# Kernel tuning notes

Hardware: AMD Instinct MI355X
Metric: run time of the kernel (lower is better)

The kernel has to match this reference:

```python
import jax, jax.numpy as jnp
import numpy as np

B, S, D, H = 4, 2048, 1024, 16
HD = D // H


def setup_inputs() -> dict:
    key = jax.random.key(0)
    ks = jax.random.split(key, 6)
    s = 1.0 / np.sqrt(D)
    return {
        "x": jax.random.normal(ks[0], (B, S, D), dtype=jnp.float32),
        "Wq": jax.random.normal(ks[1], (D, D), dtype=jnp.float32) * s,
        "Wk": jax.random.normal(ks[2], (D, D), dtype=jnp.float32) * s,
        "Wv": jax.random.normal(ks[3], (D, D), dtype=jnp.float32) * s,
        "Wo": jax.random.normal(ks[4], (D, D), dtype=jnp.float32) * s,
        "bo": jnp.zeros((D,), dtype=jnp.float32),
    }


def reference(x, Wq, Wk, Wv, Wo, bo):
    b, n, d = x.shape
    # QKV projections (torch Linear: x @ W.T, but weights here are stored as [d_in, d_out])
    q = (x @ Wq).reshape(b, n, H, HD).transpose(0, 2, 1, 3)  # [b,h,n,hd]
    k = (x @ Wk).reshape(b, n, H, HD).transpose(0, 2, 1, 3)
    v = (x @ Wv).reshape(b, n, H, HD).transpose(0, 2, 1, 3)
    scores = jnp.einsum("bhqd,bhkd->bhqk", q, k) / np.sqrt(HD)
    causal = jnp.tril(jnp.ones((n, n), dtype=bool))  # True = keep
    scores = jnp.where(causal, scores, -jnp.inf)
    attn = jax.nn.softmax(scores, axis=-1)
    ctx = jnp.einsum("bhqk,bhkd->bhqd", attn, v)
    ctx = ctx.transpose(0, 2, 1, 3).reshape(b, n, d)
    return ctx @ Wo + bo
```

## Files before the change

### kernel.cpp

```cpp
#include <hip/hip_runtime.h>
#include <hip/hip_bf16.h>

typedef __bf16 bf16;
typedef __bf16 bf16x4 __attribute__((ext_vector_type(4)));
typedef __bf16 bf16x8 __attribute__((ext_vector_type(8)));
typedef float f32x4 __attribute__((ext_vector_type(4)));

static constexpr int Bn = 4, Sn = 2048, Dn = 1024, Hn = 16, HDn = 64;
static constexpr int Mn = Bn * Sn;

__device__ __forceinline__ void gload_lds16(const void* g, void* l) {
  __builtin_amdgcn_global_load_lds(
      (const __attribute__((address_space(1))) unsigned int*)g,
      (__attribute__((address_space(3))) unsigned int*)l, 16, 0, 0);
}

struct alignas(8) B4 { bf16 e[4]; };

__global__ void prep_kernel(const float* __restrict__ x, bf16* __restrict__ xb,
                            const float* __restrict__ W0, const float* __restrict__ W1,
                            const float* __restrict__ W2, const float* __restrict__ W3,
                            bf16* __restrict__ WtQKV, bf16* __restrict__ Wot) {
  const int bid = blockIdx.x;
  if (bid < 4096) {
    const int i = bid * 256 + threadIdx.x;
    const float4* p = reinterpret_cast<const float4*>(x) + (size_t)i * 2;
    float4 a = p[0], b = p[1];
    bf16x8 v;
    v[0] = (bf16)a.x; v[1] = (bf16)a.y; v[2] = (bf16)a.z; v[3] = (bf16)a.w;
    v[4] = (bf16)b.x; v[5] = (bf16)b.y; v[6] = (bf16)b.z; v[7] = (bf16)b.w;
    *(reinterpret_cast<bf16x8*>(xb) + i) = v;
    return;
  }
  __shared__ bf16 tile[64][65];
  const int rem = bid - 4096;
  const int which = rem >> 8;
  const int by = (rem & 255) >> 4;
  const int bx = rem & 15;
  const float* W = (which == 0) ? W0 : (which == 1) ? W1 : (which == 2) ? W2 : W3;
  bf16* out = (which < 3) ? (WtQKV + (size_t)which * 1024 * 1024) : Wot;
  const int k0 = by * 64, n0 = bx * 64;
  const int t = threadIdx.x;
  const int tr = t >> 4, tc = (t & 15) * 4;
#pragma unroll
  for (int rr = 0; rr < 4; ++rr) {
    const int row = rr * 16 + tr;
    float4 v = *reinterpret_cast<const float4*>(&W[(size_t)(k0 + row) * 1024 + n0 + tc]);
    tile[row][tc + 0] = (bf16)v.x; tile[row][tc + 1] = (bf16)v.y;
    tile[row][tc + 2] = (bf16)v.z; tile[row][tc + 3] = (bf16)v.w;
  }
  __syncthreads();
#pragma unroll
  for (int rr = 0; rr < 4; ++rr) {
    const int row = rr * 16 + tr;
    B4 o;
#pragma unroll
    for (int j = 0; j < 4; ++j) o.e[j] = tile[tc + j][row];
    *reinterpret_cast<B4*>(&out[(size_t)(n0 + row) * 1024 + k0 + tc]) = o;
  }
}

template <int MODE>
__global__ __launch_bounds__(256, 4)
void gemm_kernel(const bf16* __restrict__ A, const bf16* __restrict__ Bt,
                 float* __restrict__ Co, const float* __restrict__ bias,
                 bf16* __restrict__ Qo, bf16* __restrict__ Ko, bf16* __restrict__ Vto) {
  __shared__ bf16 Al[128 * 64];
  __shared__ bf16 Bl[128 * 64];
  const int tid = threadIdx.x;
  const int lane = tid & 63;
  const int wv = tid >> 6;
  const int wm = wv >> 1, wn = wv & 1;
  const int lr = lane & 15, lg = lane >> 4;
  const int m0 = blockIdx.y * 128, n0 = blockIdx.x * 128;

  int soff[4];
  const bf16* srcA[4];
  const bf16* srcB[4];
#pragma unroll
  for (int it = 0; it < 4; ++it) {
    const int elem = it * 2048 + tid * 8;
    const int row = elem >> 6;
    const int g = (elem >> 3) & 7;
    const int gs = g ^ (row & 7);
    soff[it] = elem;
    srcA[it] = A + (size_t)(m0 + row) * 1024 + gs * 8;
    srcB[it] = Bt + (size_t)(n0 + row) * 1024 + gs * 8;
  }

  int offA[8], offB[8];
#pragma unroll
  for (int kk = 0; kk < 2; ++kk)
#pragma unroll
    for (int i = 0; i < 4; ++i) {
      const int rowA = wm * 64 + i * 16 + lr;
      offA[kk * 4 + i] = rowA * 64 + (((kk * 4 + lg) ^ (rowA & 7)) << 3);
      const int rowB = wn * 64 + i * 16 + lr;
      offB[kk * 4 + i] = rowB * 64 + (((kk * 4 + lg) ^ (rowB & 7)) << 3);
    }

  f32x4 acc[4][4] = {};

  for (int ks = 0; ks < 16; ++ks) {
    const int kn = ks * 64;
#pragma unroll
    for (int it = 0; it < 4; ++it) {
      gload_lds16(srcA[it] + kn, (bf16*)&Al[0] + soff[it]);
      gload_lds16(srcB[it] + kn, (bf16*)&Bl[0] + soff[it]);
    }
    __syncthreads();
#pragma unroll
    for (int kk = 0; kk < 2; ++kk) {
      bf16x8 af[4], bfr[4];
#pragma unroll
      for (int i = 0; i < 4; ++i) {
        af[i] = *reinterpret_cast<const bf16x8*>(Al + offA[kk * 4 + i]);
        bfr[i] = *reinterpret_cast<const bf16x8*>(Bl + offB[kk * 4 + i]);
      }
#pragma unroll
      for (int mi = 0; mi < 4; ++mi)
#pragma unroll
        for (int ni = 0; ni < 4; ++ni)
          acc[mi][ni] = __builtin_amdgcn_mfma_f32_16x16x32_bf16(af[mi], bfr[ni], acc[mi][ni], 0, 0, 0);
    }
    __syncthreads();
  }

  const int mrow = lg * 4;
  if (MODE == 0) {
    const int w = n0 >> 10;
    const int nl0 = n0 & 1023;
    if (w == 2) {
      const int b = m0 >> 11;
      const int sBase = (m0 & 2047) + wm * 64 + lg * 8;
#pragma unroll
      for (int ni = 0; ni < 4; ++ni) {
        const int nl = nl0 + wn * 64 + ni * 16 + lr;
        const int h = nl >> 6, hd = nl & 63;
        bf16* vbase = Vto + ((size_t)(b * 16 + h) * 64 + hd) * 2048;
#pragma unroll
        for (int mi = 0; mi < 4; ++mi) {
          B4 o;
#pragma unroll
          for (int i = 0; i < 4; ++i) o.e[i] = (bf16)acc[mi][ni][i];
          const int sNew = sBase + ((mi >> 1) << 5) + ((mi & 1) << 2);
          *reinterpret_cast<B4*>(&vbase[sNew]) = o;
        }
      }
    } else {
      const float fs = (w == 0) ? 0.18033688011112042f : 1.0f;
#pragma unroll
      for (int ni = 0; ni < 4; ++ni) {
        const int nl = nl0 + wn * 64 + ni * 16 + lr;
        const int h = nl >> 6, hd = nl & 63;
        bf16* dst = (w == 0) ? Qo : Ko;
#pragma unroll
        for (int mi = 0; mi < 4; ++mi) {
#pragma unroll
          for (int i = 0; i < 4; ++i) {
            const int m_g = m0 + wm * 64 + mi * 16 + mrow + i;
            const int b = m_g >> 11, s = m_g & 2047;
            dst[((size_t)(b * 16 + h) * 2048 + s) * 64 + hd] = (bf16)(acc[mi][ni][i] * fs);
          }
        }
      }
    }
  } else {
#pragma unroll
    for (int ni = 0; ni < 4; ++ni) {
      const int n_g = n0 + wn * 64 + ni * 16 + lr;
      const float bv = bias[n_g];
#pragma unroll
      for (int mi = 0; mi < 4; ++mi) {
#pragma unroll
        for (int i = 0; i < 4; ++i) {
          const int m_g = m0 + wm * 64 + mi * 16 + mrow + i;
          Co[(size_t)m_g * 1024 + n_g] = acc[mi][ni][i] + bv;
        }
      }
    }
  }
}

__device__ __forceinline__ unsigned int pack2(float lo, float hi) {
  union { bf16 bb[2]; unsigned int u; } c;
  c.bb[0] = (bf16)lo; c.bb[1] = (bf16)hi;
  return c.u;
}

template <bool DOMASK>
__device__ __forceinline__ float smax_pack(const f32x4 (&sc)[4], unsigned int (&pk)[4][2],
                                           int kv0, int qrow, int lg) {
  float p[4][4];
  float rs = 0.f;
#pragma unroll
  for (int ni = 0; ni < 4; ++ni)
#pragma unroll
    for (int r = 0; r < 4; ++r) {
      float pv = __builtin_amdgcn_exp2f(sc[ni][r]);
      if (DOMASK && (kv0 + ni * 16 + lg * 4 + r > qrow)) pv = 0.f;
      p[ni][r] = pv;
      rs += pv;
    }
#pragma unroll
  for (int ni = 0; ni < 4; ++ni)
#pragma unroll
    for (int tt = 0; tt < 2; ++tt)
      pk[ni][tt] = pack2(p[ni][2 * tt], p[ni][2 * tt + 1]);
  return rs;
}

__global__ __launch_bounds__(256, 4)
void attn_kernel(const bf16* __restrict__ Q, const bf16* __restrict__ K,
                 const bf16* __restrict__ Vt, bf16* __restrict__ ctx) {
  __shared__ bf16 Kl[2][4096];
  __shared__ bf16 Vl[2][4096];
  const int tid = threadIdx.x, lane = tid & 63, wv = tid >> 6;
  const int lr = lane & 15, lg = lane >> 4, lk = lg * 8;
  const int bid = blockIdx.x;
  const int xcd = bid & 7, slot = bid >> 3;
  const int bh = xcd * 8 + (slot >> 4);
  const int pi = slot & 15;
  const bf16* Qh = Q + (size_t)bh * Sn * 64;
  const bf16* Kh = K + (size_t)bh * Sn * 64;
  const bf16* Vh = Vt + (size_t)bh * 64 * (size_t)Sn;
  const int b = bh >> 4, h = bh & 15;

  const int e0 = tid * 8, e1 = 2048 + tid * 8;
  const int r0 = e0 >> 6, r1 = e1 >> 6;
  const int gs0 = ((e0 >> 3) & 7) ^ (r0 & 7), gs1 = ((e1 >> 3) & 7) ^ (r1 & 7);
  const bf16* srcK0 = Kh + r0 * 64 + gs0 * 8;
  const bf16* srcK1 = Kh + r1 * 64 + gs1 * 8;
  const bf16* srcV0 = Vh + (size_t)r0 * Sn + gs0 * 8;
  const bf16* srcV1 = Vh + (size_t)r1 * Sn + gs1 * 8;

  int offs[8];
#pragma unroll
  for (int kk = 0; kk < 2; ++kk)
#pragma unroll
    for (int ni = 0; ni < 4; ++ni) {
      const int row = ni * 16 + lr;
      offs[kk * 4 + ni] = row * 64 + (((kk * 4 + lg) ^ (row & 7)) << 3);
    }

  for (int ph = 0; ph < 2; ++ph) {
    const int qtile = ph ? pi : 31 - pi;
    const int qw = qtile * 64 + wv * 16;
    const int qrow = qw + lr;
    bf16x8 aq[2];
#pragma unroll
    for (int kk = 0; kk < 2; ++kk)
      aq[kk] = *reinterpret_cast<const bf16x8*>(&Qh[(size_t)(qw + lr) * 64 + kk * 32 + lk]);

    f32x4 acc[4] = {};
    float lstp = 0.f;
    const int nt = qtile + 1;

    gload_lds16(srcK0, &Kl[0][e0]);
    gload_lds16(srcK1, &Kl[0][e1]);
    gload_lds16(srcV0, &Vl[0][e0]);
    gload_lds16(srcV1, &Vl[0][e1]);

    const bf16* pK0 = srcK0 + 4096;
    const bf16* pK1 = srcK1 + 4096;
    const bf16* pV0 = srcV0 + 64;
    const bf16* pV1 = srcV1 + 64;

    for (int t = 0; t < nt; ++t) {
      const int cur = t & 1;
      if (t + 1 < nt) {
        gload_lds16(pK0, &Kl[cur ^ 1][e0]);
        gload_lds16(pK1, &Kl[cur ^ 1][e1]);
        gload_lds16(pV0, &Vl[cur ^ 1][e0]);
        gload_lds16(pV1, &Vl[cur ^ 1][e1]);
        pK0 += 4096; pK1 += 4096; pV0 += 64; pV1 += 64;
        asm volatile("s_waitcnt vmcnt(4)" ::: "memory");
      } else {
        asm volatile("s_waitcnt vmcnt(0)" ::: "memory");
      }
      __builtin_amdgcn_s_barrier();
      const int kv0 = t * 64;
      const bf16* KlF = Kl[cur];
      const bf16* VlF = Vl[cur];

      f32x4 sc[4] = {};
#pragma unroll
      for (int kk = 0; kk < 2; ++kk) {
        bf16x8 ak[4];
#pragma unroll
        for (int ni = 0; ni < 4; ++ni)
          ak[ni] = *reinterpret_cast<const bf16x8*>(KlF + offs[kk * 4 + ni]);
        __builtin_amdgcn_s_setprio(1);
#pragma unroll
        for (int ni = 0; ni < 4; ++ni)
          sc[ni] = __builtin_amdgcn_mfma_f32_16x16x32_bf16(ak[ni], aq[kk], sc[ni], 0, 0, 0);
        __builtin_amdgcn_s_setprio(0);
      }
      unsigned int pk[4][2];
      if (t == nt - 1)
        lstp += smax_pack<true>(sc, pk, kv0, qrow, lg);
      else
        lstp += smax_pack<false>(sc, pk, kv0, qrow, lg);
#pragma unroll
      for (int kk = 0; kk < 2; ++kk) {
        union { unsigned int u[4]; bf16x8 v; } ap;
#pragma unroll
        for (int w = 0; w < 4; ++w) ap.u[w] = pk[2 * kk + (w >> 1)][w & 1];
        __builtin_amdgcn_s_setprio(1);
#pragma unroll
        for (int ni = 0; ni < 4; ++ni) {
          bf16x8 av = *reinterpret_cast<const bf16x8*>(VlF + offs[kk * 4 + ni]);
          acc[ni] = __builtin_amdgcn_mfma_f32_16x16x32_bf16(av, ap.v, acc[ni], 0, 0, 0);
        }
        __builtin_amdgcn_s_setprio(0);
      }
      __builtin_amdgcn_s_barrier();
    }

    float lt = lstp;
    lt += __shfl_xor(lt, 16);
    lt += __shfl_xor(lt, 32);
    const float inv = 1.f / lt;
    bf16* cbase = ctx + (((size_t)b * Sn + qw + lr) * 16 + h) * 64;
#pragma unroll
    for (int ni = 0; ni < 4; ++ni) {
      B4 o;
#pragma unroll
      for (int r = 0; r < 4; ++r) o.e[r] = (bf16)(acc[ni][r] * inv);
      *reinterpret_cast<B4*>(cbase + ni * 16 + lg * 4) = o;
    }
    __syncthreads();
  }
}

extern "C" void kernel_launch(void* const* d_in, const int* in_sizes, int n_in,
                              void* d_out, int out_size, void* d_ws, size_t ws_size,
                              hipStream_t stream) {
  const float* x = (const float*)d_in[0];
  const float* Wq = (const float*)d_in[1];
  const float* Wk = (const float*)d_in[2];
  const float* Wv = (const float*)d_in[3];
  const float* Wo = (const float*)d_in[4];
  const float* bo = (const float*)d_in[5];

  char* ws = (char*)d_ws;
  bf16* xb    = (bf16*)(ws);
  bf16* WtQKV = (bf16*)(ws + 0x1000000);
  bf16* Wot   = (bf16*)(ws + 0x1600000);
  bf16* Qb    = (bf16*)(ws + 0x1800000);
  bf16* Kb    = (bf16*)(ws + 0x2800000);
  bf16* Vtb   = (bf16*)(ws + 0x3800000);
  bf16* ctx   = xb;

  prep_kernel<<<dim3(5120), dim3(256), 0, stream>>>(x, xb, Wq, Wk, Wv, Wo, WtQKV, Wot);
  gemm_kernel<0><<<dim3(24, 64), dim3(256), 0, stream>>>(xb, WtQKV, nullptr, nullptr, Qb, Kb, Vtb);
  attn_kernel<<<dim3(1024), dim3(256), 0, stream>>>(Qb, Kb, Vtb, ctx);
  gemm_kernel<1><<<dim3(8, 64), dim3(256), 0, stream>>>(ctx, Wot, (float*)d_out, bo,
                                                        nullptr, nullptr, nullptr);
}
```

Measured before the change: 155.4 us.

## Double-buffer QKV GEMM with 256-row tiles and 512-thread blocks

Splits the QKV projection into its own kernel with a 256x128 tile, 8 waves per block, and double-buffered LDS fed by direct global-to-LDS loads. The loads for the next K step are issued before computing the current one, using a partial vmcnt wait, and s_setprio raises priority around the MFMA block. The aim is to hide global load latency and reuse B tiles across more rows. In exchange LDS use grows to 96KB per block and there are fewer resident blocks per CU. The output projection keeps the old single-buffered kernel.

```diff
diff --git a/kernel.cpp b/kernel.cpp
--- a/kernel.cpp
+++ b/kernel.cpp
@@ -60,11 +60,134 @@
   }
 }
 
-template <int MODE>
+__global__ __launch_bounds__(512, 2)
+void gemm_qkv(const bf16* __restrict__ A, const bf16* __restrict__ Bt,
+              bf16* __restrict__ Qo, bf16* __restrict__ Ko, bf16* __restrict__ Vto) {
+  __shared__ bf16 Al[2][256 * 64];
+  __shared__ bf16 Bl[2][128 * 64];
+  const int tid = threadIdx.x;
+  const int lane = tid & 63;
+  const int wv = tid >> 6;
+  const int wm = wv >> 1, wn = wv & 1;
+  const int lr = lane & 15, lg = lane >> 4;
+  const int m0 = blockIdx.y * 256, n0 = blockIdx.x * 128;
+
+  int soffA[4];
+  const bf16* srcA[4];
+#pragma unroll
+  for (int c = 0; c < 4; ++c) {
+    const int elem = c * 4096 + tid * 8;
+    const int row = elem >> 6;
+    const int gs = ((elem >> 3) & 7) ^ (row & 7);
+    soffA[c] = elem;
+    srcA[c] = A + (size_t)(m0 + row) * 1024 + gs * 8;
+  }
+  int soffB[2];
+  const bf16* srcB[2];
+#pragma unroll
+  for (int c = 0; c < 2; ++c) {
+    const int elem = c * 4096 + tid * 8;
+    const int row = elem >> 6;
+    const int gs = ((elem >> 3) & 7) ^ (row & 7);
+    soffB[c] = elem;
+    srcB[c] = Bt + (size_t)(n0 + row) * 1024 + gs * 8;
+  }
+
+  int offA[8], offB[8];
+#pragma unroll
+  for (int kk = 0; kk < 2; ++kk)
+#pragma unroll
+    for (int i = 0; i < 4; ++i) {
+      const int rowA = wm * 64 + i * 16 + lr;
+      offA[kk * 4 + i] = rowA * 64 + (((kk * 4 + lg) ^ (rowA & 7)) << 3);
+      const int rowB = wn * 64 + i * 16 + lr;
+      offB[kk * 4 + i] = rowB * 64 + (((kk * 4 + lg) ^ (rowB & 7)) << 3);
+    }
+
+  f32x4 acc[4][4] = {};
+
+#pragma unroll
+  for (int c = 0; c < 4; ++c) gload_lds16(srcA[c], (bf16*)&Al[0][0] + soffA[c]);
+#pragma unroll
+  for (int c = 0; c < 2; ++c) gload_lds16(srcB[c], (bf16*)&Bl[0][0] + soffB[c]);
+
+  for (int ks = 0; ks < 16; ++ks) {
+    const int cur = ks & 1;
+    if (ks + 1 < 16) {
+      const int kn = (ks + 1) * 64;
+#pragma unroll
+      for (int c = 0; c < 4; ++c) gload_lds16(srcA[c] + kn, (bf16*)&Al[cur ^ 1][0] + soffA[c]);
+#pragma unroll
+      for (int c = 0; c < 2; ++c) gload_lds16(srcB[c] + kn, (bf16*)&Bl[cur ^ 1][0] + soffB[c]);
+      asm volatile("s_waitcnt vmcnt(6)" ::: "memory");
+    } else {
+      asm volatile("s_waitcnt vmcnt(0)" ::: "memory");
+    }
+    __builtin_amdgcn_s_barrier();
+    const bf16* AlF = Al[cur];
+    const bf16* BlF = Bl[cur];
+#pragma unroll
+    for (int kk = 0; kk < 2; ++kk) {
+      bf16x8 af[4], bfr[4];
+#pragma unroll
+      for (int i = 0; i < 4; ++i) {
+        af[i] = *reinterpret_cast<const bf16x8*>(AlF + offA[kk * 4 + i]);
+        bfr[i] = *reinterpret_cast<const bf16x8*>(BlF + offB[kk * 4 + i]);
+      }
+      __builtin_amdgcn_s_setprio(1);
+#pragma unroll
+      for (int mi = 0; mi < 4; ++mi)
+#pragma unroll
+        for (int ni = 0; ni < 4; ++ni)
+          acc[mi][ni] = __builtin_amdgcn_mfma_f32_16x16x32_bf16(af[mi], bfr[ni], acc[mi][ni], 0, 0, 0);
+      __builtin_amdgcn_s_setprio(0);
+    }
+    __builtin_amdgcn_s_barrier();
+  }
+
+  const int mrow = lg * 4;
+  const int w = n0 >> 10;
+  const int nl0 = n0 & 1023;
+  if (w == 2) {
+    const int b = m0 >> 11;
+    const int sBase = (m0 & 2047) + wm * 64 + lg * 8;
+#pragma unroll
+    for (int ni = 0; ni < 4; ++ni) {
+      const int nl = nl0 + wn * 64 + ni * 16 + lr;
+      const int h = nl >> 6, hd = nl & 63;
+      bf16* vbase = Vto + ((size_t)(b * 16 + h) * 64 + hd) * 2048;
+#pragma unroll
+      for (int mi = 0; mi < 4; ++mi) {
+        B4 o;
+#pragma unroll
+        for (int i = 0; i < 4; ++i) o.e[i] = (bf16)acc[mi][ni][i];
+        const int sNew = sBase + ((mi >> 1) << 5) + ((mi & 1) << 2);
+        *reinterpret_cast<B4*>(&vbase[sNew]) = o;
+      }
+    }
+  } else {
+    const float fs = (w == 0) ? 0.18033688011112042f : 1.0f;
+#pragma unroll
+    for (int ni = 0; ni < 4; ++ni) {
+      const int nl = nl0 + wn * 64 + ni * 16 + lr;
+      const int h = nl >> 6, hd = nl & 63;
+      bf16* dst = (w == 0) ? Qo : Ko;
+#pragma unroll
+      for (int mi = 0; mi < 4; ++mi) {
+#pragma unroll
+        for (int i = 0; i < 4; ++i) {
+          const int m_g = m0 + wm * 64 + mi * 16 + mrow + i;
+          const int b = m_g >> 11, s = m_g & 2047;
+          dst[((size_t)(b * 16 + h) * 2048 + s) * 64 + hd] = (bf16)(acc[mi][ni][i] * fs);
+        }
+      }
+    }
+  }
+}
+
 __global__ __launch_bounds__(256, 4)
-void gemm_kernel(const bf16* __restrict__ A, const bf16* __restrict__ Bt,
-                 float* __restrict__ Co, const float* __restrict__ bias,
-                 bf16* __restrict__ Qo, bf16* __restrict__ Ko, bf16* __restrict__ Vto) {
+void gemm_out(const bf16* __restrict__ A, const bf16* __restrict__ Bt,
+              float* __restrict__ Co, const float* __restrict__ bias) {
   __shared__ bf16 Al[128 * 64];
   __shared__ bf16 Bl[128 * 64];
   const int tid = threadIdx.x;
@@ -127,56 +250,16 @@
   }
 
   const int mrow = lg * 4;
-  if (MODE == 0) {
-    const int w = n0 >> 10;
-    const int nl0 = n0 & 1023;
-    if (w == 2) {
-      const int b = m0 >> 11;
-      const int sBase = (m0 & 2047) + wm * 64 + lg * 8;
-#pragma unroll
-      for (int ni = 0; ni < 4; ++ni) {
-        const int nl = nl0 + wn * 64 + ni * 16 + lr;
-        const int h = nl >> 6, hd = nl & 63;
-        bf16* vbase = Vto + ((size_t)(b * 16 + h) * 64 + hd) * 2048;
-#pragma unroll
-        for (int mi = 0; mi < 4; ++mi) {
-          B4 o;
-#pragma unroll
-          for (int i = 0; i < 4; ++i) o.e[i] = (bf16)acc[mi][ni][i];
-          const int sNew = sBase + ((mi >> 1) << 5) + ((mi & 1) << 2);
-          *reinterpret_cast<B4*>(&vbase[sNew]) = o;
-        }
-      }
-    } else {
-      const float fs = (w == 0) ? 0.18033688011112042f : 1.0f;
-#pragma unroll
-      for (int ni = 0; ni < 4; ++ni) {
-        const int nl = nl0 + wn * 64 + ni * 16 + lr;
-        const int h = nl >> 6, hd = nl & 63;
-        bf16* dst = (w == 0) ? Qo : Ko;
-#pragma unroll
-        for (int mi = 0; mi < 4; ++mi) {
-#pragma unroll
-          for (int i = 0; i < 4; ++i) {
-            const int m_g = m0 + wm * 64 + mi * 16 + mrow + i;
-            const int b = m_g >> 11, s = m_g & 2047;
-            dst[((size_t)(b * 16 + h) * 2048 + s) * 64 + hd] = (bf16)(acc[mi][ni][i] * fs);
-          }
-        }
-      }
-    }
-  } else {
-#pragma unroll
-    for (int ni = 0; ni < 4; ++ni) {
-      const int n_g = n0 + wn * 64 + ni * 16 + lr;
-      const float bv = bias[n_g];
-#pragma unroll
-      for (int mi = 0; mi < 4; ++mi) {
-#pragma unroll
-        for (int i = 0; i < 4; ++i) {
-          const int m_g = m0 + wm * 64 + mi * 16 + mrow + i;
-          Co[(size_t)m_g * 1024 + n_g] = acc[mi][ni][i] + bv;
-        }
+#pragma unroll
+  for (int ni = 0; ni < 4; ++ni) {
+    const int n_g = n0 + wn * 64 + ni * 16 + lr;
+    const float bv = bias[n_g];
+#pragma unroll
+    for (int mi = 0; mi < 4; ++mi) {
+#pragma unroll
+      for (int i = 0; i < 4; ++i) {
+        const int m_g = m0 + wm * 64 + mi * 16 + mrow + i;
+        Co[(size_t)m_g * 1024 + n_g] = acc[mi][ni][i] + bv;
       }
     }
   }
@@ -353,8 +436,7 @@
   bf16* ctx   = xb;
 
   prep_kernel<<<dim3(5120), dim3(256), 0, stream>>>(x, xb, Wq, Wk, Wv, Wo, WtQKV, Wot);
-  gemm_kernel<0><<<dim3(24, 64), dim3(256), 0, stream>>>(xb, WtQKV, nullptr, nullptr, Qb, Kb, Vtb);
+  gemm_qkv<<<dim3(24, 32), dim3(512), 0, stream>>>(xb, WtQKV, Qb, Kb, Vtb);
   attn_kernel<<<dim3(1024), dim3(256), 0, stream>>>(Qb, Kb, Vtb, ctx);
-  gemm_kernel<1><<<dim3(8, 64), dim3(256), 0, stream>>>(ctx, Wot, (float*)d_out, bo,
-                                                        nullptr, nullptr, nullptr);
-}
+  gemm_out<<<dim3(8, 64), dim3(256), 0, stream>>>(ctx, Wot, (float*)d_out, bo);
+}
```

Result: slower. 168.0 us (+8.2%).
